# Kernel tuning notes

Measured on AMD Instinct MI355X. Metric: run time of the kernel, lower is better.

## Reference

```python
import jax, jax.numpy as jnp
import numpy as np
import math

H = 1024
N = 64          # d_state; complex modes = N // 2
N2 = N // 2
B = 8
L = 2048
DT_MIN, DT_MAX = 0.001, 0.1


def setup_inputs() -> dict:
    key = jax.random.key(0)
    ks = jax.random.split(key, 8)
    u = jax.random.normal(ks[0], (B, H, L), dtype=jnp.float32)
    # log_dt ~ Uniform[log(dt_min), log(dt_max)]
    log_dt = (jax.random.uniform(ks[1], (H,), dtype=jnp.float32)
              * (math.log(DT_MAX) - math.log(DT_MIN)) + math.log(DT_MIN))
    # random_dplr with scaling='inverse': real part 0.5, imag = (1/pi)*N*(N/(1+2n)-1)
    n = jnp.arange(N2, dtype=jnp.float32)
    w_real = 0.5 * jnp.ones((1, N2), dtype=jnp.float32)
    w_imag = ((1.0 / math.pi) * N * (N / (1.0 + 2.0 * n) - 1.0))[None, :].astype(jnp.float32)
    log_w_real = jnp.log(w_real + 1e-4)  # module stores log(-w.real + 1e-4)
    # C = randn complex (channels=1, H, N2), scaled by normalized B (folded into randn here)
    C_re = jax.random.normal(ks[2], (1, H, N2), dtype=jnp.float32) / math.sqrt(2 * N2)
    C_im = jax.random.normal(ks[3], (1, H, N2), dtype=jnp.float32) / math.sqrt(2 * N2)
    D = jax.random.normal(ks[4], (1, H), dtype=jnp.float32)
    # output_linear: Conv1d(k=1) from channels*H -> H  => weight (H, H)
    W_out = jax.random.normal(ks[5], (H, H), dtype=jnp.float32) / math.sqrt(H)
    b_out = jax.random.normal(ks[6], (H,), dtype=jnp.float32) * 0.01
    return {"u": u, "log_dt": log_dt, "log_w_real": log_w_real, "w_imag": w_imag,
            "C_re": C_re, "C_im": C_im, "D": D, "W_out": W_out, "b_out": b_out}


def reference(u, log_dt, log_w_real, w_imag, C_re, C_im, D, W_out, b_out):
    b, h, l = u.shape
    # --- SSKernelDiag.forward ---
    dt = jnp.exp(log_dt)                                   # (H,)
    w = -jnp.exp(log_w_real) + 1j * w_imag                 # (n_ssm=1, N2)
    w = jnp.broadcast_to(w, (h, w.shape[-1]))              # repeat copies -> (H, N2)
    dtA = w * dt[:, None]                                  # (H, N2) complex
    C = (C_re + 1j * C_im) * (jnp.exp(dtA) - 1.0) / w      # (c, H, N2)
    # Vandermonde: exp(dtA * arange(L)) -> (H, N2, L) complex
    K = jnp.exp(dtA[:, :, None] * jnp.arange(l, dtype=jnp.float32))
    k = 2.0 * jnp.einsum('chn,hnl->chl', C, K).real        # (c, H, L) float
    # --- FFT convolution ---
    k_f = jnp.fft.rfft(k, n=2 * l)                         # (c, H, L+1)
    u_f = jnp.fft.rfft(u, n=2 * l)                         # (B, H, L+1)
    y_f = jnp.einsum('bhl,chl->bchl', u_f, k_f)
    y = jnp.fft.irfft(y_f, n=2 * l)[..., :l]               # (B, c, H, L)
    # skip connection with D
    y = y + jnp.einsum('bhl,ch->bchl', u, D)
    y = y.reshape(b, -1, l)                                # (B, c*H, L)
    y = jax.nn.gelu(y, approximate=False)
    # output 1x1 conv: (B, c*H, L) x (H, c*H) -> (B, H, L)
    y = jnp.einsum('bil,oi->bol', y, W_out) + b_out[None, :, None]
    return y
```

## Files before the change

### kernel.cpp

```cpp
#include <hip/hip_runtime.h>
#include <hip/hip_bf16.h>

#define HH 1024
#define LL 2048
#define BB 8
#define NN2 32
#define CT 128
#define NCH 16

typedef short bf16x8 __attribute__((ext_vector_type(8)));
typedef float f32x4  __attribute__((ext_vector_type(4)));

static __device__ __forceinline__ unsigned short bfbits(float x) {
    __hip_bfloat16 h = __float2bfloat16(x);
    return *(unsigned short*)&h;
}
static __device__ __forceinline__ float f_from_bits(unsigned short b) {
    __hip_bfloat16 h; *(unsigned short*)&h = b; return __bfloat162float(h);
}
static __device__ __forceinline__ float2 cexp_n(float2 dA, float p) {
    float mag = __expf(dA.x * p);
    float rev = dA.y * p * 0.15915494309f;
    rev -= floorf(rev);
    float ang = rev * 6.28318530718f;
    return make_float2(mag * __cosf(ang), mag * __sinf(ang));
}

#define S_U    0
#define S_UN   16384
#define S_P    32768
#define S_KT   40960
#define S_DTA  41472
#define S_CN   41728
#define S_TOT  41984

#define SWZ(off, row) ((off) ^ (((row) & 7) << 4))

__global__ __launch_bounds__(512, 6) void ssm_mfma(
    const float* __restrict__ u, const float* __restrict__ log_dt,
    const float* __restrict__ log_w_real, const float* __restrict__ w_imag,
    const float* __restrict__ C_re, const float* __restrict__ C_im,
    const float* __restrict__ Dp, __hip_bfloat16* __restrict__ g_out)
{
    extern __shared__ char smem[];
    float2* dtA = (float2*)(smem + S_DTA);
    float2* Cn  = (float2*)(smem + S_CN);
    float*  kt  = (float*)(smem + S_KT);

    const int tid  = threadIdx.x;
    const int lane = tid & 63;
    const int wave = tid >> 6;
    const int wm   = wave >> 2;
    const int wn   = wave & 3;
    const int h    = blockIdx.x;
    const int bh   = blockIdx.y;

    float4 ureg[4];
    #pragma unroll
    for (int q = 0; q < 4; ++q) {
        int b = bh * 4 + q;
        ureg[q] = *(const float4*)(u + ((size_t)(b * HH + h)) * LL + tid * 4);
    }
    if (tid < NN2) {
        int n = tid;
        float dt = expf(log_dt[h]);
        float wr = -expf(log_w_real[n]);
        float wi = w_imag[n];
        float dar = wr * dt, dai = wi * dt;
        dtA[n] = make_float2(dar, dai);
        float er = expf(dar);
        float sn, cs; sincosf(dai, &sn, &cs);
        float exr = er * cs - 1.0f, exi = er * sn;
        float den = wr * wr + wi * wi;
        float fr = (exr * wr + exi * wi) / den;
        float fi = (exi * wr - exr * wi) / den;
        float cre = C_re[h * NN2 + n], cim = C_im[h * NN2 + n];
        Cn[n] = make_float2(cre * fr - cim * fi, cre * fi + cim * fr);
    }
    __syncthreads();

    #pragma unroll
    for (int q = 0; q < 4; ++q) {
        int row = q * 16 + (tid >> 5);
        int j   = (tid & 31) * 4;
        ushort4 o;
        o.x = bfbits(ureg[q].x); o.y = bfbits(ureg[q].y);
        o.z = bfbits(ureg[q].z); o.w = bfbits(ureg[q].w);
        *(ushort4*)(smem + SWZ(S_U + row * 256 + j * 2, row)) = o;
    }
    #pragma unroll
    for (int q = 0; q < 2; ++q) {
        int vidx = q * 512 + tid;
        int n = vidx >> 5, j0 = (vidx & 31) * 4;
        float2 dA = dtA[n];
        float2 a0 = cexp_n(dA, (float)(127 - j0));
        float2 a1 = cexp_n(dA, (float)(126 - j0));
        float2 a2 = cexp_n(dA, (float)(125 - j0));
        float2 a3 = cexp_n(dA, (float)(124 - j0));
        ushort4 re, im;
        re.x = bfbits(a0.x); re.y = bfbits(a1.x); re.z = bfbits(a2.x); re.w = bfbits(a3.x);
        im.x = bfbits(a0.y); im.y = bfbits(a1.y); im.z = bfbits(a2.y); im.w = bfbits(a3.y);
        int r0 = 2 * n, r1 = 2 * n + 1;
        *(ushort4*)(smem + SWZ(S_UN + r0 * 256 + j0 * 2, r0)) = re;
        *(ushort4*)(smem + SWZ(S_UN + r1 * 256 + j0 * 2, r1)) = im;
    }
    {
        int t = tid >> 2, nb = (tid & 3) * 8;
        float s = 0.f;
        #pragma unroll
        for (int i = 0; i < 8; ++i) {
            int n = nb + i;
            float2 a = cexp_n(dtA[n], (float)t);
            float2 C = Cn[n];
            s += C.x * a.x - C.y * a.y;
        }
        s += __shfl_xor(s, 1);
        s += __shfl_xor(s, 2);
        if ((tid & 3) == 0) kt[t] = 2.0f * s;
    }
    __syncthreads();

    f32x4 accP[2] = {};
    #pragma unroll
    for (int ks = 0; ks < 4; ++ks) {
        int kf = ks * 32 + (lane >> 4) * 8;
        bf16x8 a0, a1, b0;
        {
            int r = wm * 32 + (lane & 15);
            a0 = *(bf16x8*)(smem + SWZ(S_U + r * 256 + kf * 2, r));
            int r2 = r + 16;
            a1 = *(bf16x8*)(smem + SWZ(S_U + r2 * 256 + kf * 2, r2));
        }
        {
            int r = wn * 16 + (lane & 15);
            b0 = *(bf16x8*)(smem + SWZ(S_UN + r * 256 + kf * 2, r));
        }
        accP[0] = __builtin_amdgcn_mfma_f32_16x16x32_bf16(a0, b0, accP[0], 0, 0, 0);
        accP[1] = __builtin_amdgcn_mfma_f32_16x16x32_bf16(a1, b0, accP[1], 0, 0, 0);
    }
    #pragma unroll
    for (int mt = 0; mt < 2; ++mt)
        #pragma unroll
        for (int r = 0; r < 4; ++r) {
            int row = wm * 32 + mt * 16 + (lane >> 4) * 4 + r;
            int col = wn * 16 + (lane & 15);
            *(unsigned short*)(smem + SWZ(S_P + row * 128 + col * 2, row)) =
                bfbits(accP[mt][r]);
        }
    __syncthreads();

    #pragma unroll
    for (int q = 0; q < 16; ++q) {
        int idx = q * 512 + tid;
        int ttr = idx >> 6, j = idx & 63;
        float val = (ttr >= j) ? kt[ttr - j] : 0.0f;
        *(unsigned short*)(smem + SWZ(S_UN + ttr * 128 + j * 2, ttr)) = bfbits(val);
    }
    if (tid < 128) {
        int b = tid >> 5, n = tid & 31;
        float2 C = Cn[n];
        float2 A = cexp_n(dtA[n], 128.0f);
        float sr = 0.f, si = 0.f;
        for (int c = 0; c < NCH; ++c) {
            int row = b * 16 + c;
            int off = SWZ(S_P + row * 128 + n * 4, row);
            unsigned int pv = *(unsigned int*)(smem + off);
            float pr = f_from_bits((unsigned short)(pv & 0xffff));
            float pi = f_from_bits((unsigned short)(pv >> 16));
            float csr = C.x * sr - C.y * si;
            float csi = C.x * si + C.y * sr;
            *(unsigned int*)(smem + off) =
                (unsigned)bfbits(csr) | ((unsigned)bfbits(csi) << 16);
            float nsr = A.x * sr - A.y * si + pr;
            float nsi = A.x * si + A.y * sr + pi;
            sr = nsr; si = nsi;
        }
    }
    __syncthreads();

    f32x4 acc[2][2] = {};
    #pragma unroll
    for (int ks = 0; ks < 2; ++ks) {
        int kf = ks * 32 + (lane >> 4) * 8;
        bf16x8 a0, a1, bv[2];
        {
            int r = wm * 32 + (lane & 15);
            a0 = *(bf16x8*)(smem + SWZ(S_U + r * 256 + kf * 2, r));
            int r2 = r + 16;
            a1 = *(bf16x8*)(smem + SWZ(S_U + r2 * 256 + kf * 2, r2));
        }
        #pragma unroll
        for (int nt = 0; nt < 2; ++nt) {
            int ttr = wn * 32 + nt * 16 + (lane & 15);
            bv[nt] = *(bf16x8*)(smem + SWZ(S_UN + ttr * 128 + kf * 2, ttr));
        }
        #pragma unroll
        for (int nt = 0; nt < 2; ++nt) {
            acc[0][nt] = __builtin_amdgcn_mfma_f32_16x16x32_bf16(a0, bv[nt], acc[0][nt], 0, 0, 0);
            acc[1][nt] = __builtin_amdgcn_mfma_f32_16x16x32_bf16(a1, bv[nt], acc[1][nt], 0, 0, 0);
        }
    }
    __syncthreads();

    #pragma unroll
    for (int q = 0; q < 16; ++q) {
        int idx = q * 512 + tid;
        int ttr = idx >> 6, j = idx & 63;
        float val = (ttr >= 64 + j) ? kt[ttr - 64 - j] : 0.0f;
        *(unsigned short*)(smem + SWZ(S_UN + ttr * 128 + j * 2, ttr)) = bfbits(val);
    }
    __syncthreads();
    #pragma unroll
    for (int ks = 0; ks < 2; ++ks) {
        int kf = ks * 32 + (lane >> 4) * 8;
        bf16x8 a0, a1, bv[2];
        {
            int r = wm * 32 + (lane & 15);
            a0 = *(bf16x8*)(smem + SWZ(S_U + r * 256 + 128 + kf * 2, r));
            int r2 = r + 16;
            a1 = *(bf16x8*)(smem + SWZ(S_U + r2 * 256 + 128 + kf * 2, r2));
        }
        #pragma unroll
        for (int nt = 0; nt < 2; ++nt) {
            int ttr = wn * 32 + nt * 16 + (lane & 15);
            bv[nt] = *(bf16x8*)(smem + SWZ(S_UN + ttr * 128 + kf * 2, ttr));
        }
        #pragma unroll
        for (int nt = 0; nt < 2; ++nt) {
            acc[0][nt] = __builtin_amdgcn_mfma_f32_16x16x32_bf16(a0, bv[nt], acc[0][nt], 0, 0, 0);
            acc[1][nt] = __builtin_amdgcn_mfma_f32_16x16x32_bf16(a1, bv[nt], acc[1][nt], 0, 0, 0);
        }
    }
    __syncthreads();

    #pragma unroll
    for (int q = 0; q < 8; ++q) {
        int idx = q * 512 + tid;
        int n = idx >> 7, ttr = idx & 127;
        float2 a = cexp_n(dtA[n], (float)(ttr + 1));
        int off = SWZ(S_UN + ttr * 128 + n * 4, ttr);
        *(unsigned int*)(smem + off) =
            (unsigned)bfbits(2.0f * a.x) | ((unsigned)bfbits(-2.0f * a.y) << 16);
    }
    __syncthreads();
    #pragma unroll
    for (int ks = 0; ks < 2; ++ks) {
        int kf = ks * 32 + (lane >> 4) * 8;
        bf16x8 a0, a1, bv[2];
        {
            int r = wm * 32 + (lane & 15);
            a0 = *(bf16x8*)(smem + SWZ(S_P + r * 128 + kf * 2, r));
            int r2 = r + 16;
            a1 = *(bf16x8*)(smem + SWZ(S_P + r2 * 128 + kf * 2, r2));
        }
        #pragma unroll
        for (int nt = 0; nt < 2; ++nt) {
            int ttr = wn * 32 + nt * 16 + (lane & 15);
            bv[nt] = *(bf16x8*)(smem + SWZ(S_UN + ttr * 128 + kf * 2, ttr));
        }
        #pragma unroll
        for (int nt = 0; nt < 2; ++nt) {
            acc[0][nt] = __builtin_amdgcn_mfma_f32_16x16x32_bf16(a0, bv[nt], acc[0][nt], 0, 0, 0);
            acc[1][nt] = __builtin_amdgcn_mfma_f32_16x16x32_bf16(a1, bv[nt], acc[1][nt], 0, 0, 0);
        }
    }

    const float Dv = Dp[h];
    #pragma unroll
    for (int mt = 0; mt < 2; ++mt)
        #pragma unroll
        for (int nt = 0; nt < 2; ++nt)
            #pragma unroll
            for (int r = 0; r < 4; ++r) {
                int row = wm * 32 + mt * 16 + (lane >> 4) * 4 + r;
                int ttr = wn * 32 + nt * 16 + (lane & 15);
                int off = SWZ(S_U + row * 256 + ttr * 2, row);
                float uv = f_from_bits(*(unsigned short*)(smem + off));
                float y = acc[mt][nt][r] + Dv * uv;
                float z = 0.7978845608f * (y + 0.044715f * y * y * y);
                float e = __expf(2.0f * z);
                float th = 1.0f - 2.0f / (e + 1.0f);
                float gel = 0.5f * y * (1.0f + th);
                *(unsigned short*)(smem + off) = bfbits(gel);
            }
    __syncthreads();
    #pragma unroll
    for (int q = 0; q < 2; ++q) {
        int flat = q * 512 + tid;
        int row = flat >> 4, c16 = flat & 15;
        uint4 v = *(uint4*)(smem + SWZ(S_U + row * 256 + c16 * 16, row));
        int b = bh * 4 + (row >> 4), c = row & 15;
        *(uint4*)(g_out + ((size_t)(b * HH + h)) * LL + c * CT + c16 * 8) = v;
    }
}

__global__ __launch_bounds__(256) void conv_w(
    const float* __restrict__ W, __hip_bfloat16* __restrict__ Wb)
{
    int i = blockIdx.x * 256 + threadIdx.x;
    float4 v = ((const float4*)W)[i];
    ushort4 o;
    o.x = bfbits(v.x); o.y = bfbits(v.y); o.z = bfbits(v.z); o.w = bfbits(v.w);
    ((ushort4*)Wb)[i] = o;
}

__global__ __launch_bounds__(256) void transpose_g(
    const __hip_bfloat16* __restrict__ g, __hip_bfloat16* __restrict__ gT)
{
    __shared__ __hip_bfloat16 t[64][66];
    const int tid = threadIdx.x;
    const int b  = blockIdx.z;
    const int h0 = blockIdx.x * 64;
    const int l0 = blockIdx.y * 64;

    #pragma unroll
    for (int q = 0; q < 2; ++q) {
        int idx = tid + q * 256;
        int r = idx >> 3, c8 = (idx & 7) * 8;
        uint4 v = *(const uint4*)(g + ((size_t)(b * HH + h0 + r)) * LL + l0 + c8);
        unsigned int* dst = (unsigned int*)&t[r][c8];
        dst[0] = v.x; dst[1] = v.y; dst[2] = v.z; dst[3] = v.w;
    }
    __syncthreads();
    #pragma unroll
    for (int q = 0; q < 2; ++q) {
        int idx = tid + q * 256;
        int r = idx >> 3, c8 = (idx & 7) * 8;
        unsigned short tmp[8];
        #pragma unroll
        for (int j = 0; j < 8; ++j) tmp[j] = *(unsigned short*)&t[c8 + j][r];
        uint4 o;
        o.x = (unsigned)tmp[0] | ((unsigned)tmp[1] << 16);
        o.y = (unsigned)tmp[2] | ((unsigned)tmp[3] << 16);
        o.z = (unsigned)tmp[4] | ((unsigned)tmp[5] << 16);
        o.w = (unsigned)tmp[6] | ((unsigned)tmp[7] << 16);
        *(uint4*)(gT + ((size_t)(b * LL + l0 + r)) * HH + h0 + c8) = o;
    }
}

#define GSLOT 32768
#define STAGE_TILE(kt_, s_)                                                      \
    {                                                                            \
        const int k0_ = (kt_) * 64;                                              \
        _Pragma("unroll")                                                        \
        for (int v_ = 0; v_ < 4; ++v_) {                                         \
            int row_ = v_ * 64 + rsub;                                           \
            const __hip_bfloat16* ga_ = Wb + (size_t)(o0 + row_) * HH + k0_ + csw; \
            const __hip_bfloat16* gb_ = gT + (size_t)(n0 + row_) * HH + k0_ + csw; \
            char* dA_ = smem + (s_) * GSLOT + (v_ * 64 + wave * 8) * 128;        \
            char* dB_ = smem + 2 * GSLOT + (s_) * GSLOT + (v_ * 64 + wave * 8) * 128; \
            __builtin_amdgcn_global_load_lds(                                    \
                (const __attribute__((address_space(1))) void*)ga_,              \
                (__attribute__((address_space(3))) void*)dA_, 16, 0, 0);         \
            __builtin_amdgcn_global_load_lds(                                    \
                (const __attribute__((address_space(1))) void*)gb_,              \
                (__attribute__((address_space(3))) void*)dB_, 16, 0, 0);         \
        }                                                                        \
    }

#define COMPUTE_TILE(s_)                                                         \
    {                                                                            \
        const char* baseA = smem + (s_) * GSLOT;                                 \
        const char* baseB = smem + 2 * GSLOT + (s_) * GSLOT;                     \
        bf16x8 bfr[4][2];                                                        \
        _Pragma("unroll")                                                        \
        for (int nt = 0; nt < 4; ++nt)                                           \
            _Pragma("unroll")                                                    \
            for (int ks = 0; ks < 2; ++ks) {                                     \
                int rb = wn * 64 + nt * 16 + (lane & 15);                        \
                int c  = (ks * 32 + (lane >> 4) * 8) ^ ((rb & 7) << 3);          \
                bfr[nt][ks] = *(const bf16x8*)(baseB + rb * 128 + c * 2);        \
            }                                                                    \
        _Pragma("unroll")                                                        \
        for (int qq = 0; qq < 4; ++qq) {                                         \
            bf16x8 af[2][2];                                                     \
            _Pragma("unroll")                                                    \
            for (int mt = 0; mt < 2; ++mt)                                       \
                _Pragma("unroll")                                                \
                for (int ks = 0; ks < 2; ++ks) {                                 \
                    int ra = wm * 128 + (qq * 2 + mt) * 16 + (lane & 15);        \
                    int c  = (ks * 32 + (lane >> 4) * 8) ^ ((ra & 7) << 3);      \
                    af[mt][ks] = *(const bf16x8*)(baseA + ra * 128 + c * 2);     \
                }                                                                \
            __builtin_amdgcn_s_setprio(1);                                       \
            _Pragma("unroll")                                                    \
            for (int mt = 0; mt < 2; ++mt)                                       \
                _Pragma("unroll")                                                \
                for (int nt = 0; nt < 4; ++nt) {                                 \
                    acc[qq * 2 + mt][nt] = __builtin_amdgcn_mfma_f32_16x16x32_bf16( \
                        af[mt][0], bfr[nt][0], acc[qq * 2 + mt][nt], 0, 0, 0);   \
                    acc[qq * 2 + mt][nt] = __builtin_amdgcn_mfma_f32_16x16x32_bf16( \
                        af[mt][1], bfr[nt][1], acc[qq * 2 + mt][nt], 0, 0, 0);   \
                }                                                                \
            __builtin_amdgcn_s_setprio(0);                                       \
        }                                                                        \
    }

__global__ __launch_bounds__(512, 2) void out_gemm_256(
    const __hip_bfloat16* __restrict__ Wb,
    const __hip_bfloat16* __restrict__ gT,
    const float* __restrict__ bias,
    float* __restrict__ out)
{
    extern __shared__ char smem[];
    const int tid  = threadIdx.x;
    const int lane = tid & 63;
    const int wave = tid >> 6;
    const int wm = wave >> 2;
    const int wn = wave & 3;

    int wg  = blockIdx.x;
    int swz = (wg & 7) * 32 + (wg >> 3);
    const int o0 = (swz & 3) * 256;
    const int n0 = (swz >> 2) * 256;

    const int rsub = tid >> 3;
    const int csw  = ((tid & 7) ^ (rsub & 7)) << 3;

    f32x4 acc[8][4] = {};

    STAGE_TILE(0, 0)
    STAGE_TILE(1, 1)

    for (int t = 0; t < 15; ++t) {
        asm volatile("s_waitcnt vmcnt(8)" ::: "memory");
        __builtin_amdgcn_s_barrier();
        __builtin_amdgcn_sched_barrier(0);
        COMPUTE_TILE(t & 1)
        asm volatile("s_waitcnt lgkmcnt(0)" ::: "memory");
        __builtin_amdgcn_s_barrier();
        __builtin_amdgcn_sched_barrier(0);
        if (t < 14) STAGE_TILE(t + 2, t & 1)
    }
    asm volatile("s_waitcnt vmcnt(0)" ::: "memory");
    __builtin_amdgcn_s_barrier();
    __builtin_amdgcn_sched_barrier(0);
    COMPUTE_TILE(1)

    const int bb = n0 >> 11;
    #pragma unroll
    for (int m = 0; m < 8; ++m) {
        int o = o0 + wm * 128 + m * 16 + (lane >> 4) * 4;
        #pragma unroll
        for (int nt = 0; nt < 4; ++nt) {
            int n = n0 + wn * 64 + nt * 16 + (lane & 15);
            int l = n & 2047;
            #pragma unroll
            for (int r = 0; r < 4; ++r)
                out[((size_t)(bb * HH + o + r)) * LL + l] = acc[m][nt][r] + bias[o + r];
        }
    }
}

extern "C" void kernel_launch(void* const* d_in, const int* in_sizes, int n_in,
                              void* d_out, int out_size, void* d_ws, size_t ws_size,
                              hipStream_t stream) {
    const float* u          = (const float*)d_in[0];
    const float* log_dt     = (const float*)d_in[1];
    const float* log_w_real = (const float*)d_in[2];
    const float* w_imag     = (const float*)d_in[3];
    const float* C_re       = (const float*)d_in[4];
    const float* C_im       = (const float*)d_in[5];
    const float* Dp         = (const float*)d_in[6];
    const float* W          = (const float*)d_in[7];
    const float* bias       = (const float*)d_in[8];
    float* out = (float*)d_out;

    __hip_bfloat16* g  = (__hip_bfloat16*)d_out;
    __hip_bfloat16* gT = (__hip_bfloat16*)d_ws;
    __hip_bfloat16* Wb = (__hip_bfloat16*)((char*)d_ws + 33554432);

    hipFuncSetAttribute((const void*)ssm_mfma,
                        hipFuncAttributeMaxDynamicSharedMemorySize, S_TOT);
    hipFuncSetAttribute((const void*)out_gemm_256,
                        hipFuncAttributeMaxDynamicSharedMemorySize, 131072);

    conv_w<<<dim3(HH * HH / 1024), 256, 0, stream>>>(W, Wb);
    ssm_mfma<<<dim3(HH, 2), 512, S_TOT, stream>>>(u, log_dt, log_w_real, w_imag,
                                                  C_re, C_im, Dp, g);
    transpose_g<<<dim3(HH / 64, LL / 64, BB), 256, 0, stream>>>(g, gT);
    out_gemm_256<<<dim3(256), 512, 131072, stream>>>(Wb, gT, bias, out);
}
```

Measured before the change: 114.3 us.

## Precompute per-channel SSM tables in separate kernel and stream into LDS

Adds an aux_tables kernel that computes, once per channel, the Vandermonde tables, the kernel taps, the C coefficients and A^128 in bf16/fp32 and writes them to global scratch. The main SSM kernel then copies these with global_load_lds instead of recomputing transcendentals in each of its two batch-half blocks. The Toeplitz build is also vectorized to four bf16 values per store. This trades duplicated exp/sin/cos work for an extra launch and global traffic, and places scratch tables in the output buffer, which assumes g is later overwritten.

```diff
diff --git a/kernel.cpp b/kernel.cpp
--- a/kernel.cpp
+++ b/kernel.cpp
@@ -26,26 +26,125 @@
     return make_float2(mag * __cosf(ang), mag * __sinf(ang));
 }
 
+#define SWZ(off, row) ((off) ^ (((row) & 7) << 4))
+
+__global__ __launch_bounds__(256) void aux_tables(
+    const float* __restrict__ log_dt, const float* __restrict__ log_w_real,
+    const float* __restrict__ w_imag, const float* __restrict__ C_re,
+    const float* __restrict__ C_im,
+    __hip_bfloat16* __restrict__ AJ_g, __hip_bfloat16* __restrict__ AP_g,
+    float* __restrict__ misc_g)
+{
+    __shared__ float2 dtA_s[NN2];
+    __shared__ float2 Cn_s[NN2];
+    const int tid = threadIdx.x;
+    const int h = blockIdx.x;
+
+    if (tid < NN2) {
+        int n = tid;
+        float dt = expf(log_dt[h]);
+        float wr = -expf(log_w_real[n]);
+        float wi = w_imag[n];
+        float dar = wr * dt, dai = wi * dt;
+        dtA_s[n] = make_float2(dar, dai);
+        float er = expf(dar);
+        float sn, cs; sincosf(dai, &sn, &cs);
+        float exr = er * cs - 1.0f, exi = er * sn;
+        float den = wr * wr + wi * wi;
+        float fr = (exr * wr + exi * wi) / den;
+        float fi = (exi * wr - exr * wi) / den;
+        float cre = C_re[h * NN2 + n], cim = C_im[h * NN2 + n];
+        float2 Cv = make_float2(cre * fr - cim * fi, cre * fi + cim * fr);
+        Cn_s[n] = Cv;
+        misc_g[h * 256 + 128 + 2 * n]     = Cv.x;
+        misc_g[h * 256 + 128 + 2 * n + 1] = Cv.y;
+        float magA = expf(dar * 128.0f);
+        float snA, csA; sincosf(dai * 128.0f, &snA, &csA);
+        misc_g[h * 256 + 192 + 2 * n]     = magA * csA;
+        misc_g[h * 256 + 192 + 2 * n + 1] = magA * snA;
+    }
+    __syncthreads();
+
+    char* ajb = (char*)AJ_g + (size_t)h * 16384;
+    #pragma unroll
+    for (int q = 0; q < 2; ++q) {
+        int task = q * 256 + tid;
+        int n = task >> 4, j0 = (task & 15) * 8;
+        float2 dA = dtA_s[n];
+        unsigned rw[4], iw[4];
+        #pragma unroll
+        for (int i2 = 0; i2 < 4; ++i2) {
+            float2 a0 = cexp_n(dA, (float)(127 - j0 - 2 * i2));
+            float2 a1 = cexp_n(dA, (float)(127 - j0 - 2 * i2 - 1));
+            rw[i2] = (unsigned)bfbits(a0.x) | ((unsigned)bfbits(a1.x) << 16);
+            iw[i2] = (unsigned)bfbits(a0.y) | ((unsigned)bfbits(a1.y) << 16);
+        }
+        int r0 = 2 * n, r1 = 2 * n + 1;
+        *(uint4*)(ajb + SWZ(r0 * 256 + j0 * 2, r0)) = make_uint4(rw[0], rw[1], rw[2], rw[3]);
+        *(uint4*)(ajb + SWZ(r1 * 256 + j0 * 2, r1)) = make_uint4(iw[0], iw[1], iw[2], iw[3]);
+    }
+
+    char* apb = (char*)AP_g + (size_t)h * 16384;
+    #pragma unroll
+    for (int q = 0; q < 2; ++q) {
+        int task = q * 256 + tid;
+        int ttr = task >> 2, n0 = (task & 3) * 8;
+        unsigned w[8];
+        #pragma unroll
+        for (int i = 0; i < 8; ++i) {
+            float2 a = cexp_n(dtA_s[n0 + i], (float)(ttr + 1));
+            w[i] = (unsigned)bfbits(2.0f * a.x) | ((unsigned)bfbits(-2.0f * a.y) << 16);
+        }
+        *(uint4*)(apb + SWZ(ttr * 128 + n0 * 4, ttr))      = make_uint4(w[0], w[1], w[2], w[3]);
+        *(uint4*)(apb + SWZ(ttr * 128 + n0 * 4 + 16, ttr)) = make_uint4(w[4], w[5], w[6], w[7]);
+    }
+
+    {
+        int t = tid >> 1, nb = (tid & 1) * 16;
+        float s = 0.f;
+        #pragma unroll
+        for (int i = 0; i < 16; ++i) {
+            int n = nb + i;
+            float2 a = cexp_n(dtA_s[n], (float)t);
+            float2 C = Cn_s[n];
+            s += C.x * a.x - C.y * a.y;
+        }
+        s += __shfl_xor(s, 1);
+        if ((tid & 1) == 0) misc_g[h * 256 + t] = 2.0f * s;
+    }
+}
+
 #define S_U    0
 #define S_UN   16384
 #define S_P    32768
 #define S_KT   40960
-#define S_DTA  41472
-#define S_CN   41728
 #define S_TOT  41984
 
-#define SWZ(off, row) ((off) ^ (((row) & 7) << 4))
+#define KBUILD(hf)                                                       \
+    _Pragma("unroll")                                                    \
+    for (int q = 0; q < 4; ++q) {                                        \
+        int idx = q * 512 + tid;                                         \
+        int ttr = idx >> 4, j0 = (idx & 15) * 4;                         \
+        int base = ttr - (hf) * 64 - j0;                                 \
+        ushort4 o;                                                       \
+        o.x = (base     >= 0) ? bfbits(kt[base])     : (unsigned short)0;\
+        o.y = (base - 1 >= 0) ? bfbits(kt[base - 1]) : (unsigned short)0;\
+        o.z = (base - 2 >= 0) ? bfbits(kt[base - 2]) : (unsigned short)0;\
+        o.w = (base - 3 >= 0) ? bfbits(kt[base - 3]) : (unsigned short)0;\
+        *(ushort4*)(smem + SWZ(S_UN + ttr * 128 + j0 * 2, ttr)) = o;     \
+    }
 
 __global__ __launch_bounds__(512, 6) void ssm_mfma(
-    const float* __restrict__ u, const float* __restrict__ log_dt,
-    const float* __restrict__ log_w_real, const float* __restrict__ w_imag,
-    const float* __restrict__ C_re, const float* __restrict__ C_im,
+    const float* __restrict__ u,
+    const __hip_bfloat16* __restrict__ AJ_g,
+    const __hip_bfloat16* __restrict__ AP_g,
+    const float* __restrict__ misc_g,
     const float* __restrict__ Dp, __hip_bfloat16* __restrict__ g_out)
 {
     extern __shared__ char smem[];
-    float2* dtA = (float2*)(smem + S_DTA);
-    float2* Cn  = (float2*)(smem + S_CN);
-    float*  kt  = (float*)(smem + S_KT);
+    float*  kt   = (float*)(smem + S_KT);
+    float2* CnL  = (float2*)(smem + S_KT + 512);
+    float2* A128 = (float2*)(smem + S_KT + 768);
 
     const int tid  = threadIdx.x;
     const int lane = tid & 63;
@@ -55,30 +154,28 @@
     const int h    = blockIdx.x;
     const int bh   = blockIdx.y;
 
+    {
+        const char* ajs = (const char*)AJ_g + (size_t)h * 16384;
+        __builtin_amdgcn_global_load_lds(
+            (const __attribute__((address_space(1))) void*)(ajs + tid * 16),
+            (__attribute__((address_space(3))) void*)(smem + S_UN + wave * 1024), 16, 0, 0);
+        __builtin_amdgcn_global_load_lds(
+            (const __attribute__((address_space(1))) void*)(ajs + 8192 + tid * 16),
+            (__attribute__((address_space(3))) void*)(smem + S_UN + 8192 + wave * 1024), 16, 0, 0);
+        if (tid < 64) {
+            const char* ms = (const char*)misc_g + (size_t)h * 1024;
+            __builtin_amdgcn_global_load_lds(
+                (const __attribute__((address_space(1))) void*)(ms + tid * 16),
+                (__attribute__((address_space(3))) void*)(smem + S_KT), 16, 0, 0);
+        }
+    }
+
     float4 ureg[4];
     #pragma unroll
     for (int q = 0; q < 4; ++q) {
         int b = bh * 4 + q;
         ureg[q] = *(const float4*)(u + ((size_t)(b * HH + h)) * LL + tid * 4);
     }
-    if (tid < NN2) {
-        int n = tid;
-        float dt = expf(log_dt[h]);
-        float wr = -expf(log_w_real[n]);
-        float wi = w_imag[n];
-        float dar = wr * dt, dai = wi * dt;
-        dtA[n] = make_float2(dar, dai);
-        float er = expf(dar);
-        float sn, cs; sincosf(dai, &sn, &cs);
-        float exr = er * cs - 1.0f, exi = er * sn;
-        float den = wr * wr + wi * wi;
-        float fr = (exr * wr + exi * wi) / den;
-        float fi = (exi * wr - exr * wi) / den;
-        float cre = C_re[h * NN2 + n], cim = C_im[h * NN2 + n];
-        Cn[n] = make_float2(cre * fr - cim * fi, cre * fi + cim * fr);
-    }
-    __syncthreads();
-
     #pragma unroll
     for (int q = 0; q < 4; ++q) {
         int row = q * 16 + (tid >> 5);
@@ -88,36 +185,7 @@
         o.z = bfbits(ureg[q].z); o.w = bfbits(ureg[q].w);
         *(ushort4*)(smem + SWZ(S_U + row * 256 + j * 2, row)) = o;
     }
-    #pragma unroll
-    for (int q = 0; q < 2; ++q) {
-        int vidx = q * 512 + tid;
-        int n = vidx >> 5, j0 = (vidx & 31) * 4;
-        float2 dA = dtA[n];
-        float2 a0 = cexp_n(dA, (float)(127 - j0));
-        float2 a1 = cexp_n(dA, (float)(126 - j0));
-        float2 a2 = cexp_n(dA, (float)(125 - j0));
-        float2 a3 = cexp_n(dA, (float)(124 - j0));
-        ushort4 re, im;
-        re.x = bfbits(a0.x); re.y = bfbits(a1.x); re.z = bfbits(a2.x); re.w = bfbits(a3.x);
-        im.x = bfbits(a0.y); im.y = bfbits(a1.y); im.z = bfbits(a2.y); im.w = bfbits(a3.y);
-        int r0 = 2 * n, r1 = 2 * n + 1;
-        *(ushort4*)(smem + SWZ(S_UN + r0 * 256 + j0 * 2, r0)) = re;
-        *(ushort4*)(smem + SWZ(S_UN + r1 * 256 + j0 * 2, r1)) = im;
-    }
-    {
-        int t = tid >> 2, nb = (tid & 3) * 8;
-        float s = 0.f;
-        #pragma unroll
-        for (int i = 0; i < 8; ++i) {
-            int n = nb + i;
-            float2 a = cexp_n(dtA[n], (float)t);
-            float2 C = Cn[n];
-            s += C.x * a.x - C.y * a.y;
-        }
-        s += __shfl_xor(s, 1);
-        s += __shfl_xor(s, 2);
-        if ((tid & 3) == 0) kt[t] = 2.0f * s;
-    }
+    asm volatile("s_waitcnt vmcnt(0)" ::: "memory");
     __syncthreads();
 
     f32x4 accP[2] = {};
@@ -149,17 +217,11 @@
         }
     __syncthreads();
 
-    #pragma unroll
-    for (int q = 0; q < 16; ++q) {
-        int idx = q * 512 + tid;
-        int ttr = idx >> 6, j = idx & 63;
-        float val = (ttr >= j) ? kt[ttr - j] : 0.0f;
-        *(unsigned short*)(smem + SWZ(S_UN + ttr * 128 + j * 2, ttr)) = bfbits(val);
-    }
+    KBUILD(0)
     if (tid < 128) {
         int b = tid >> 5, n = tid & 31;
-        float2 C = Cn[n];
-        float2 A = cexp_n(dtA[n], 128.0f);
+        float2 C = CnL[n];
+        float2 A = A128[n];
         float sr = 0.f, si = 0.f;
         for (int c = 0; c < NCH; ++c) {
             int row = b * 16 + c;
@@ -202,13 +264,7 @@
     }
     __syncthreads();
 
-    #pragma unroll
-    for (int q = 0; q < 16; ++q) {
-        int idx = q * 512 + tid;
-        int ttr = idx >> 6, j = idx & 63;
-        float val = (ttr >= 64 + j) ? kt[ttr - 64 - j] : 0.0f;
-        *(unsigned short*)(smem + SWZ(S_UN + ttr * 128 + j * 2, ttr)) = bfbits(val);
-    }
+    KBUILD(1)
     __syncthreads();
     #pragma unroll
     for (int ks = 0; ks < 2; ++ks) {
@@ -233,16 +289,18 @@
     }
     __syncthreads();
 
-    #pragma unroll
-    for (int q = 0; q < 8; ++q) {
-        int idx = q * 512 + tid;
-        int n = idx >> 7, ttr = idx & 127;
-        float2 a = cexp_n(dtA[n], (float)(ttr + 1));
-        int off = SWZ(S_UN + ttr * 128 + n * 4, ttr);
-        *(unsigned int*)(smem + off) =
-            (unsigned)bfbits(2.0f * a.x) | ((unsigned)bfbits(-2.0f * a.y) << 16);
-    }
-    __syncthreads();
+    {
+        const char* aps = (const char*)AP_g + (size_t)h * 16384;
+        __builtin_amdgcn_global_load_lds(
+            (const __attribute__((address_space(1))) void*)(aps + tid * 16),
+            (__attribute__((address_space(3))) void*)(smem + S_UN + wave * 1024), 16, 0, 0);
+        __builtin_amdgcn_global_load_lds(
+            (const __attribute__((address_space(1))) void*)(aps + 8192 + tid * 16),
+            (__attribute__((address_space(3))) void*)(smem + S_UN + 8192 + wave * 1024), 16, 0, 0);
+    }
+    asm volatile("s_waitcnt vmcnt(0)" ::: "memory");
+    __syncthreads();
+
     #pragma unroll
     for (int ks = 0; ks < 2; ++ks) {
         int kf = ks * 32 + (lane >> 4) * 8;
@@ -466,9 +524,12 @@
     const float* bias       = (const float*)d_in[8];
     float* out = (float*)d_out;
 
-    __hip_bfloat16* g  = (__hip_bfloat16*)d_out;
-    __hip_bfloat16* gT = (__hip_bfloat16*)d_ws;
-    __hip_bfloat16* Wb = (__hip_bfloat16*)((char*)d_ws + 33554432);
+    __hip_bfloat16* AJ_g = (__hip_bfloat16*)d_out;
+    __hip_bfloat16* AP_g = (__hip_bfloat16*)((char*)d_out + 16777216);
+    __hip_bfloat16* g    = (__hip_bfloat16*)((char*)d_out + 33554432);
+    __hip_bfloat16* gT     = (__hip_bfloat16*)d_ws;
+    __hip_bfloat16* Wb     = (__hip_bfloat16*)((char*)d_ws + 33554432);
+    float*          misc_g = (float*)((char*)d_ws + 35651584);
 
     hipFuncSetAttribute((const void*)ssm_mfma,
                         hipFuncAttributeMaxDynamicSharedMemorySize, S_TOT);
@@ -476,8 +537,9 @@
                         hipFuncAttributeMaxDynamicSharedMemorySize, 131072);
 
     conv_w<<<dim3(HH * HH / 1024), 256, 0, stream>>>(W, Wb);
-    ssm_mfma<<<dim3(HH, 2), 512, S_TOT, stream>>>(u, log_dt, log_w_real, w_imag,
-                                                  C_re, C_im, Dp, g);
+    aux_tables<<<dim3(HH), 256, 0, stream>>>(log_dt, log_w_real, w_imag,
+                                             C_re, C_im, AJ_g, AP_g, misc_g);
+    ssm_mfma<<<dim3(HH, 2), 512, S_TOT, stream>>>(u, AJ_g, AP_g, misc_g, Dp, g);
     transpose_g<<<dim3(HH / 64, LL / 64, BB), 256, 0, stream>>>(g, gT);
     out_gemm_256<<<dim3(256), 512, 131072, stream>>>(Wb, gT, bias, out);
 }
```

After: 108.4 us. 5.1% less time.
